# Kernel optimization log

Hardware: AMD Instinct MI355X
Metric: run time of the kernel (lower is better)

Reference implementation:

```python
import jax, jax.numpy as jnp
import numpy as np

BATCH = 2
TIME_N = 196
SPACE_F = 8
D_MODEL = 768
N_HEADS = 12
D_STATE = 16
DT_RANK = 48  # ceil(768/16)
D_CONV = 4
SEQ = 1 + TIME_N * SPACE_F


def _ln(x, w, b, eps=1e-5):
    m = x.mean(-1, keepdims=True)
    v = ((x - m) ** 2).mean(-1, keepdims=True)
    return (x - m) * jax.lax.rsqrt(v + eps) * w + b


def _silu(x):
    return x * jax.nn.sigmoid(x)


def _causal_conv(x, w, b):
    # x: (B, L, d); depthwise causal conv1d, kernel D_CONV, padding left
    L = x.shape[1]
    xp = jnp.pad(x, ((0, 0), (D_CONV - 1, 0), (0, 0)))
    return sum(xp[:, k:k + L, :] * w[:, k] for k in range(D_CONV)) + b


def _ssm(u, delta, A, Bm, C, Dp):
    # u, delta: (B,L,d); A: (d,N); Bm, C: (B,L,N)
    dA = jnp.exp(delta[..., None] * A)                    # (B,L,d,N)
    dBu = (delta * u)[..., None] * Bm[:, :, None, :]      # (B,L,d,N)
    B, L, d, N = dA.shape

    def step(h, inp):
        a, bu = inp
        h = a * h + bu
        return h, h

    _, hs = jax.lax.scan(step, jnp.zeros((B, d, N), dA.dtype),
                         (dA.transpose(1, 0, 2, 3), dBu.transpose(1, 0, 2, 3)))
    return jnp.einsum('lbdn,bln->bld', hs, C) + u * Dp


def _mamba_dir(xp, z, conv_w, conv_b, xproj_w, dt_w, dt_b, A_log, Dp, flip):
    if flip:
        xp = xp[:, ::-1]
        z = z[:, ::-1]
    xc = _silu(_causal_conv(xp, conv_w, conv_b))
    x_dbl = xc @ xproj_w.T
    dt = x_dbl[..., :DT_RANK]
    Bm = x_dbl[..., DT_RANK:DT_RANK + D_STATE]
    C = x_dbl[..., DT_RANK + D_STATE:]
    delta = jax.nn.softplus(dt @ dt_w.T + dt_b)
    y = _ssm(xc, delta, -jnp.exp(A_log), Bm, C, Dp) * _silu(z)
    if flip:
        y = y[:, ::-1]
    return y


def _mamba(x, in_w, cw, cb, xw, dw, db, Al, Dp, cwb, cbb, xwb, dwb, dbb, Alb, Dpb, out_w):
    # bimamba v2: forward scan + backward (flipped) scan, summed, then out_proj
    xz = x @ in_w.T
    xp, z = jnp.split(xz, 2, axis=-1)
    y = (_mamba_dir(xp, z, cw, cb, xw, dw, db, Al, Dp, False)
         + _mamba_dir(xp, z, cwb, cbb, xwb, dwb, dbb, Alb, Dpb, True))
    return y @ out_w.T


def _mha(x, in_w, in_b, out_w, out_b):
    # torch nn.MultiheadAttention default (batch_first=False):
    # x is (L, N, E); attention runs over dim 0 (L), dim 1 (N) is batch.
    L, N, E = x.shape
    hd = E // N_HEADS
    qkv = x @ in_w.T + in_b
    q, k, v = jnp.split(qkv, 3, axis=-1)
    q = q.reshape(L, N, N_HEADS, hd)
    k = k.reshape(L, N, N_HEADS, hd)
    v = v.reshape(L, N, N_HEADS, hd)
    scores = jnp.einsum('lnhk,mnhk->nhlm', q, k) / jnp.sqrt(jnp.asarray(hd, x.dtype))
    o = jnp.einsum('nhlm,mnhk->lnhk', jax.nn.softmax(scores, axis=-1), v)
    return o.reshape(L, N, E) @ out_w.T + out_b


def _forward(x, norm1_w, norm1_b, norm2_w, norm2_b, norm3_w, norm3_b,
             attn_in_w, attn_in_b, attn_out_w, attn_out_b,
             m_in_w, m_conv_w, m_conv_b, m_xproj_w, m_dt_w, m_dt_b, m_Alog, m_D,
             m_conv_wb, m_conv_bb, m_xproj_wb, m_dt_wb, m_dt_bb, m_Alog_b, m_D_b,
             m_out_w, fc1_w, fc1_b, fc2_w, fc2_b, time_n, space_f):
    b, _, d = x.shape
    init_cls = x[:, :1]
    res_x = x
    # 'b (n t) d -> (b n) t d'
    xt = x[:, 1:].reshape(b, time_n, space_f, d).reshape(b * time_n, space_f, d)
    time_out = _mamba(_ln(xt, norm3_w, norm3_b), m_in_w, m_conv_w, m_conv_b,
                      m_xproj_w, m_dt_w, m_dt_b, m_Alog, m_D,
                      m_conv_wb, m_conv_bb, m_xproj_wb, m_dt_wb, m_dt_bb,
                      m_Alog_b, m_D_b, m_out_w)
    time_res = (xt + time_out).reshape(b, time_n, space_f, d)
    # cls repeat: 'b t d -> (b t) 1 d'
    cls = jnp.repeat(init_cls, space_f, axis=1).reshape(b * space_f, 1, d)
    # 'b (n t) d -> (b t) n d'
    xs = time_res.transpose(0, 2, 1, 3).reshape(b * space_f, time_n, d)
    xs = jnp.concatenate([cls, xs], axis=1)  # (b*t, n+1, d)
    space_out = _mha(_ln(xs, norm1_w, norm1_b), attn_in_w, attn_in_b, attn_out_w, attn_out_b)
    cls_tok = space_out[:, 0].reshape(b, space_f, d).mean(1, keepdims=True)
    # '(b t) n d -> b (n t) d'
    sp = space_out[:, 1:].reshape(b, space_f, time_n, d).transpose(0, 2, 1, 3).reshape(b, time_n * space_f, d)
    x = res_x + jnp.concatenate([cls_tok, sp], axis=1)
    h = _ln(x, norm2_w, norm2_b)
    h = jax.nn.gelu(h @ fc1_w.T + fc1_b, approximate=False) @ fc2_w.T + fc2_b
    return x + h


def setup_inputs():
    ks = iter(jax.random.split(jax.random.key(0), 64))

    def nrm(shape, s=0.02):
        return jax.random.normal(next(ks), shape, dtype=jnp.float32) * s

    d = D_MODEL
    Alog = jnp.log(jnp.tile(jnp.arange(1, D_STATE + 1, dtype=jnp.float32), (d, 1)))
    return dict(
        x=jax.random.normal(next(ks), (BATCH, SEQ, d), dtype=jnp.float32),
        norm1_w=jnp.ones((d,), jnp.float32), norm1_b=jnp.zeros((d,), jnp.float32),
        norm2_w=jnp.ones((d,), jnp.float32), norm2_b=jnp.zeros((d,), jnp.float32),
        norm3_w=jnp.ones((d,), jnp.float32), norm3_b=jnp.zeros((d,), jnp.float32),
        attn_in_w=nrm((3 * d, d)), attn_in_b=nrm((3 * d,)),
        attn_out_w=nrm((d, d)), attn_out_b=nrm((d,)),
        m_in_w=nrm((2 * d, d)),
        m_conv_w=nrm((d, D_CONV), 0.2), m_conv_b=nrm((d,), 0.1),
        m_xproj_w=nrm((DT_RANK + 2 * D_STATE, d)),
        m_dt_w=nrm((d, DT_RANK), 0.1), m_dt_b=nrm((d,), 0.5),
        m_Alog=Alog, m_D=jnp.ones((d,), jnp.float32),
        m_conv_wb=nrm((d, D_CONV), 0.2), m_conv_bb=nrm((d,), 0.1),
        m_xproj_wb=nrm((DT_RANK + 2 * D_STATE, d)),
        m_dt_wb=nrm((d, DT_RANK), 0.1), m_dt_bb=nrm((d,), 0.5),
        m_Alog_b=Alog, m_D_b=jnp.ones((d,), jnp.float32),
        m_out_w=nrm((d, d)),
        fc1_w=nrm((4 * d, d)), fc1_b=nrm((4 * d,), 0.01),
        fc2_w=nrm((d, 4 * d)), fc2_b=nrm((d,), 0.01),
        time_n=TIME_N, space_f=SPACE_F,
    )


def reference(x, norm1_w, norm1_b, norm2_w, norm2_b, norm3_w, norm3_b,
              attn_in_w, attn_in_b, attn_out_w, attn_out_b,
              m_in_w, m_conv_w, m_conv_b, m_xproj_w, m_dt_w, m_dt_b, m_Alog, m_D,
              m_conv_wb, m_conv_bb, m_xproj_wb, m_dt_wb, m_dt_bb, m_Alog_b, m_D_b,
              m_out_w, fc1_w, fc1_b, fc2_w, fc2_b, time_n, space_f):
    return _forward(x, norm1_w, norm1_b, norm2_w, norm2_b, norm3_w, norm3_b,
                    attn_in_w, attn_in_b, attn_out_w, attn_out_b,
                    m_in_w, m_conv_w, m_conv_b, m_xproj_w, m_dt_w, m_dt_b, m_Alog, m_D,
                    m_conv_wb, m_conv_bb, m_xproj_wb, m_dt_wb, m_dt_bb, m_Alog_b, m_D_b,
                    m_out_w, fc1_w, fc1_b, fc2_w, fc2_b, time_n, space_f)
```

## Files before the change

kernel.cpp:

```cpp
#include <hip/hip_runtime.h>
#include <hip/hip_bf16.h>
#include <math.h>

#define DM 768
#define NBATCH 2
#define TIMEN 196
#define SPACEF 8
#define SEQL 1569
#define NSTATE 16
#define MT 3136
#define NSEQ 392
#define AT 3152
#define XTOK 3138

typedef __attribute__((ext_vector_type(8))) short s16x8;
typedef __attribute__((ext_vector_type(4))) float f32x4;
typedef __hip_bfloat16 bf16;

__device__ __forceinline__ float silu_fast(float x){ return __fdividef(x, 1.0f + __expf(-x)); }
__device__ __forceinline__ float geluf(float x){
  float y = 0.7978845608f * (x + 0.044715f*x*x*x);
  float ay = fabsf(y);
  float e = __expf(-2.0f*ay);
  float t = __fdividef(1.0f - e, 1.0f + e);
  t = copysignf(t, y);
  return 0.5f*x*(1.0f + t);
}
__device__ __forceinline__ float softplusf(float x){
  return (x > 20.0f) ? x : __logf(1.0f + __expf(x));
}
__device__ __forceinline__ int imin(int a, int b){ return a < b ? a : b; }

#define GLD_LDS16(g, l) __builtin_amdgcn_global_load_lds( \
    (const __attribute__((address_space(1))) void*)(g), \
    (__attribute__((address_space(3))) void*)(l), 16, 0, 0)

template<int N, int K, int Np, int Kp>
__device__ __forceinline__ void cvt_seg(const float* __restrict__ src, bf16* __restrict__ dst){
  const int total = Np * Kp;
  int base = blockIdx.x * 1024 + threadIdx.x;
  #pragma unroll
  for (int e = 0; e < 4; e++){
    int idx = base + e * 256;
    if (idx < total){
      int n = idx / Kp, k = idx % Kp;
      float v = (n < N && k < K) ? src[n * K + k] : 0.0f;
      dst[idx] = __float2bfloat16(v);
    }
  }
}

__global__ __launch_bounds__(256) void cvtw_kernel(
    const float* s0, const float* s1, const float* s2, const float* s3,
    const float* s4, const float* s5, const float* s6, const float* s7,
    const float* s8, const float* s9, bf16* w)
{
  switch (blockIdx.y) {
    case 0: cvt_seg<1536,768,1536,768>(s0, w + 0);        break;
    case 1: cvt_seg<  80,768, 128,768>(s1, w + 1179648);  break;
    case 2: cvt_seg<  80,768, 128,768>(s2, w + 1277952);  break;
    case 3: cvt_seg< 768, 48, 768, 64>(s3, w + 1376256);  break;
    case 4: cvt_seg< 768, 48, 768, 64>(s4, w + 1425408);  break;
    case 5: cvt_seg< 768,768, 768,768>(s5, w + 1474560);  break;
    case 6: cvt_seg<2304,768,2304,768>(s6, w + 2064384);  break;
    case 7: cvt_seg< 768,768, 768,768>(s7, w + 3833856);  break;
    case 8: cvt_seg<3072,768,3072,768>(s8, w + 4423680);  break;
    default:cvt_seg< 768,3072,768,3072>(s9, w + 6782976); break;
  }
}

__device__ __forceinline__ float block_sum256(float v, float* sm){
  #pragma unroll
  for (int o = 32; o > 0; o >>= 1) v += __shfl_down(v, o);
  __syncthreads();
  if ((threadIdx.x & 63) == 0) sm[threadIdx.x >> 6] = v;
  __syncthreads();
  return sm[0] + sm[1] + sm[2] + sm[3];
}

__global__ __launch_bounds__(256) void ln_kernel(
    const float* __restrict__ src0,
    const float* __restrict__ w, const float* __restrict__ b,
    bf16* __restrict__ out)
{
  __shared__ float sm[4];
  int tok = blockIdx.x;
  int bi = tok / (TIMEN*SPACEF), r = tok % (TIMEN*SPACEF);
  const float* src = src0 + ((size_t)bi * SEQL + 1 + r) * DM;
  int tid = threadIdx.x;
  float xr[3];
  #pragma unroll
  for (int i = 0; i < 3; i++) xr[i] = src[tid + i*256];
  float mean = block_sum256(xr[0]+xr[1]+xr[2], sm) * (1.0f/768.0f);
  float v0 = xr[0]-mean, v1 = xr[1]-mean, v2 = xr[2]-mean;
  float var = block_sum256(v0*v0 + v1*v1 + v2*v2, sm) * (1.0f/768.0f);
  float rstd = rsqrtf(var + 1e-5f);
  bf16* o = out + (size_t)tok * DM;
  #pragma unroll
  for (int i = 0; i < 3; i++){ int c = tid + i*256;
    o[c] = __float2bfloat16((xr[i]-mean)*rstd*w[c] + b[c]); }
}

__global__ __launch_bounds__(256) void redk_ln(
    const float* __restrict__ part, const float* __restrict__ x,
    const float* __restrict__ w, const float* __restrict__ b,
    bf16* __restrict__ out)
{
  __shared__ float sm[4];
  int tok = blockIdx.x;
  int sidx = tok / 197, p = tok % 197;
  int tid = threadIdx.x;
  float xr[3];
  if (p == 0) {
    const float* src = x + (size_t)(sidx >> 3) * SEQL * DM;
    #pragma unroll
    for (int i = 0; i < 3; i++) xr[i] = src[tid + i*256];
  } else {
    int bi = sidx >> 3, f = sidx & 7, t = p - 1;
    size_t mt = ((size_t)(bi*TIMEN + t))*SPACEF + f;
    const float* p0 = part + mt*DM;
    const float* p1 = part + ((size_t)MT + mt)*DM;
    const float* xs = x + ((size_t)bi*SEQL + 1 + t*SPACEF + f)*DM;
    #pragma unroll
    for (int i = 0; i < 3; i++){ int c = tid + i*256;
      xr[i] = p0[c] + p1[c] + xs[c]; }
  }
  float mean = block_sum256(xr[0]+xr[1]+xr[2], sm) * (1.0f/768.0f);
  float v0 = xr[0]-mean, v1 = xr[1]-mean, v2 = xr[2]-mean;
  float var = block_sum256(v0*v0 + v1*v1 + v2*v2, sm) * (1.0f/768.0f);
  float rstd = rsqrtf(var + 1e-5f);
  bf16* o = out + (size_t)tok * DM;
  #pragma unroll
  for (int i = 0; i < 3; i++){ int c = tid + i*256;
    o[c] = __float2bfloat16((xr[i]-mean)*rstd*w[c] + b[c]); }
}

__global__ __launch_bounds__(256) void scatter_ln(
    const float* __restrict__ part, const float* __restrict__ bias,
    const float* __restrict__ x, float* __restrict__ xnew,
    const float* __restrict__ w, const float* __restrict__ b,
    bf16* __restrict__ out)
{
  __shared__ float sm[4];
  int tok = blockIdx.x;
  int bi = tok / SEQL, row = tok % SEQL;
  int tid = threadIdx.x;
  const float* p1 = part + (size_t)AT*DM;
  const float* xs = x + (size_t)tok*DM;
  float xr[3];
  if (row == 0) {
    #pragma unroll
    for (int i = 0; i < 3; i++){ int c = tid + i*256;
      float acc = 0.0f;
      #pragma unroll
      for (int f = 0; f < SPACEF; f++){
        size_t r = ((size_t)(bi*SPACEF + f)*197)*DM + c;
        acc += part[r] + p1[r];
      }
      xr[i] = xs[c] + acc * 0.125f + bias[c];
    }
  } else {
    int t = (row - 1) >> 3, f = (row - 1) & 7;
    size_t r = ((size_t)((bi*SPACEF + f)*197) + 1 + t)*DM;
    #pragma unroll
    for (int i = 0; i < 3; i++){ int c = tid + i*256;
      xr[i] = xs[c] + part[r + c] + p1[r + c] + bias[c];
    }
  }
  float* xo = xnew + (size_t)tok*DM;
  #pragma unroll
  for (int i = 0; i < 3; i++) xo[tid + i*256] = xr[i];
  float mean = block_sum256(xr[0]+xr[1]+xr[2], sm) * (1.0f/768.0f);
  float v0 = xr[0]-mean, v1 = xr[1]-mean, v2 = xr[2]-mean;
  float var = block_sum256(v0*v0 + v1*v1 + v2*v2, sm) * (1.0f/768.0f);
  float rstd = rsqrtf(var + 1e-5f);
  bf16* o = out + (size_t)tok*DM;
  #pragma unroll
  for (int i = 0; i < 3; i++){ int c = tid + i*256;
    o[c] = __float2bfloat16((xr[i]-mean)*rstd*w[c] + b[c]); }
}

template<int BM, int BN>
__global__ __launch_bounds__(256) void mgemm(
    const bf16* __restrict__ A, int lda,
    const bf16* __restrict__ W0, const bf16* __restrict__ W1, int ldw,
    const float* __restrict__ bias0, const float* __restrict__ bias1,
    const float* __restrict__ resid,
    void* __restrict__ Cout, int M, int mhalf, int N, int ldc, int KP,
    int act, int resmode, int outbf16, int skw)
{
  constexpr int WM = BM/2, WN = BN/2, MI = WM/16, NJ = WN/16;
  __shared__ bf16 As[2][BM*64];
  __shared__ bf16 Bs[2][BN*64];
  int tid = threadIdx.x;
  int wave = tid >> 6, lane = tid & 63;

  int gx = gridDim.x, gy = gridDim.y;
  int nwg = gx * gy;
  int bid = blockIdx.y * gx + blockIdx.x;
  int m0, n0;
  if ((gx & 3) == 0 && (gy & 1) == 0) {
    int cw = gx >> 2, rh = gy >> 1;
    int xcd = bid & 7, lidx = bid >> 3;
    int rx = xcd & 3, ry = xcd >> 2;
    m0 = ((ry * rh) + lidx / cw) * BM;
    n0 = ((rx * cw) + lidx % cw) * BN;
  } else {
    int q = nwg >> 3, r = nwg & 7;
    int xcd = bid & 7, lidx = bid >> 3;
    int wg = (xcd < r ? xcd*(q+1) : r*(q+1) + (xcd-r)*q) + lidx;
    m0 = (wg / gx) * BM; n0 = (wg % gx) * BN;
  }

  int wr = wave >> 1, wc = wave & 1;

  int koff = blockIdx.z * KP;
  const bf16* Ak = A + koff;
  const bf16* Wt = ((m0 < mhalf) ? W0 : W1) + koff;
  const float* bias = (m0 < mhalf) ? bias0 : bias1;

  f32x4 acc[MI][NJ];
  #pragma unroll
  for (int i = 0; i < MI; i++)
    #pragma unroll
    for (int j = 0; j < NJ; j++) acc[i][j] = (f32x4){0.f,0.f,0.f,0.f};

  int sr8 = lane >> 3;
  int scs = (((lane & 7) ^ sr8) * 8);
  int lr16 = lane & 15, ks = (lane >> 4) * 8;
  int swz = (lr16 & 7) << 3;

  auto stage = [&](int buf, int k0){
    #pragma unroll
    for (int g = 0; g < BM/32; g++){
      int rr = wave*(BM/4) + g*8;
      const bf16* ga = Ak + (size_t)imin(m0 + rr + sr8, M-1)*lda + k0 + scs;
      GLD_LDS16(ga, &As[buf][rr*64]);
    }
    #pragma unroll
    for (int g = 0; g < BN/32; g++){
      int rr = wave*(BN/4) + g*8;
      const bf16* gb = Wt + (size_t)(n0 + rr + sr8)*ldw + k0 + scs;
      GLD_LDS16(gb, &Bs[buf][rr*64]);
    }
  };

  auto compute = [&](int buf){
    s16x8 afr[2][MI], bfr[2][NJ];
    #pragma unroll
    for (int kk = 0; kk < 2; kk++){
      #pragma unroll
      for (int i = 0; i < MI; i++)
        afr[kk][i] = *(const s16x8*)&As[buf][(wr*WM + i*16 + lr16)*64 + ((kk*32 + ks) ^ swz)];
      #pragma unroll
      for (int j = 0; j < NJ; j++)
        bfr[kk][j] = *(const s16x8*)&Bs[buf][(wc*WN + j*16 + lr16)*64 + ((kk*32 + ks) ^ swz)];
    }
    #pragma unroll
    for (int kk = 0; kk < 2; kk++)
      #pragma unroll
      for (int i = 0; i < MI; i++)
        #pragma unroll
        for (int j = 0; j < NJ; j++)
          acc[i][j] = __builtin_amdgcn_mfma_f32_16x16x32_bf16(afr[kk][i], bfr[kk][j], acc[i][j], 0, 0, 0);
  };

  stage(0, 0);
  __syncthreads();
  int cur = 0;
  for (int k0 = 64; k0 < KP; k0 += 64){
    stage(cur ^ 1, k0);
    compute(cur);
    __syncthreads();
    cur ^= 1;
  }
  compute(cur);

  #pragma unroll
  for (int i = 0; i < MI; i++){
    int rowb = m0 + wr*WM + i*16 + (lane >> 4)*4;
    #pragma unroll
    for (int j = 0; j < NJ; j++){
      int col = n0 + wc*WN + j*16 + lr16;
      if (col >= N) continue;
      float bv = bias ? bias[col] : 0.0f;
      #pragma unroll
      for (int r2 = 0; r2 < 4; r2++){
        int row = rowb + r2;
        if (row >= M) continue;
        float v = acc[i][j][r2];
        if (skw > 1){
          ((float*)Cout)[((size_t)(blockIdx.z*M) + row)*ldc + col] = v;
          continue;
        }
        v += bv;
        if (act == 1) v = geluf(v);
        else if (act == 2) v = softplusf(v);
        if (resmode == 1) v += resid[(size_t)row*ldc + col];
        if (outbf16) ((bf16*)Cout)[(size_t)row*ldc + col] = __float2bfloat16(v);
        else         ((float*)Cout)[(size_t)row*ldc + col] = v;
      }
    }
  }
}

__global__ __launch_bounds__(256) void redk(
    const float* __restrict__ part, const float* __restrict__ bias,
    const float* __restrict__ resid, float* __restrict__ out,
    int M, int sk)
{
  int i = blockIdx.x*256 + threadIdx.x;
  if (i*4 >= M*768) return;
  int row = i / 192;
  int c4 = (i - row*192) * 4;
  size_t base = (size_t)row*768 + c4;
  float4 v = *(const float4*)(part + base);
  for (int z = 1; z < sk; z++){
    float4 p = *(const float4*)(part + (size_t)z*M*768 + base);
    v.x += p.x; v.y += p.y; v.z += p.z; v.w += p.w;
  }
  float4 bvec = *(const float4*)(bias + c4);
  float4 r = *(const float4*)(resid + base);
  v.x += bvec.x + r.x; v.y += bvec.y + r.y; v.z += bvec.z + r.z; v.w += bvec.w + r.w;
  *(float4*)(out + base) = v;
}

__global__ __launch_bounds__(256) void conv_kernel(
    const float* __restrict__ xz,
    const float* __restrict__ wf, const float* __restrict__ bf,
    const float* __restrict__ wb, const float* __restrict__ bb,
    bf16* __restrict__ xcf, bf16* __restrict__ xcb)
{
  int g = blockIdx.x*256 + threadIdx.x;
  if (g >= NSEQ*DM) return;
  int s = g / DM, d = g % DM;
  float xr[8];
  #pragma unroll
  for (int j = 0; j < 8; j++) xr[j] = xz[(size_t)(s*8 + j)*1536 + d];
  float wfv[4], wbv[4];
  #pragma unroll
  for (int k = 0; k < 4; k++){ wfv[k] = wf[d*4+k]; wbv[k] = wb[d*4+k]; }
  float bfv = bf[d], bbv = bb[d];
  #pragma unroll
  for (int l = 0; l < 8; l++) {
    float af = bfv, ab = bbv;
    #pragma unroll
    for (int k = 0; k < 4; k++) {
      if (l + k >= 3) {
        af += wfv[k] * xr[l + k - 3];
        ab += wbv[k] * xr[10 - l - k];
      }
    }
    xcf[(size_t)(s*8 + l)*DM + d] = __float2bfloat16(silu_fast(af));
    xcb[(size_t)(s*8 + l)*DM + d] = __float2bfloat16(silu_fast(ab));
  }
}

__global__ __launch_bounds__(256) void ssm_kernel(
    const float* __restrict__ xz,
    const bf16* __restrict__ xcf, const bf16* __restrict__ xcb,
    const bf16* __restrict__ dblf, const bf16* __restrict__ dblb,
    const bf16* __restrict__ dlf, const bf16* __restrict__ dlb,
    const float* __restrict__ Alogf, const float* __restrict__ Df,
    const float* __restrict__ Alogb, const float* __restrict__ Db,
    bf16* __restrict__ y)
{
  int s = blockIdx.y;
  int d = blockIdx.x*256 + threadIdx.x;
  int tid = threadIdx.x;
  __shared__ float sBC[2][8][32];
  #pragma unroll
  for (int i = 0; i < 2; i++){
    int idx = tid + i*256;
    int dir = idx >> 8, r = idx & 255, l = r >> 5, j = r & 31;
    const bf16* p = dir ? dblb : dblf;
    sBC[dir][l][j] = __bfloat162float(p[(size_t)(s*8 + l)*80 + 48 + j]);
  }
  float Af[NSTATE], Ab[NSTATE];
  #pragma unroll
  for (int n = 0; n < NSTATE; n++) {
    Af[n] = -__expf(Alogf[d*NSTATE + n]);
    Ab[n] = -__expf(Alogb[d*NSTATE + n]);
  }
  float Dfv = Df[d], Dbv = Db[d];
  __syncthreads();

  float hf[NSTATE] = {}, hb[NSTATE] = {};
  float yf[8], yb[8];
  #pragma unroll
  for (int l = 0; l < 8; l++) {
    int t = s*8 + l;
    float delf = __bfloat162float(dlf[(size_t)t*DM + d]);
    float uf   = __bfloat162float(xcf[(size_t)t*DM + d]);
    float duf  = delf * uf;
    float accf = 0.0f;
    #pragma unroll
    for (int n = 0; n < NSTATE; n++) {
      hf[n] = __expf(delf*Af[n])*hf[n] + duf*sBC[0][l][n];
      accf += hf[n]*sBC[0][l][16+n];
    }
    yf[l] = accf + uf*Dfv;
    float delb = __bfloat162float(dlb[(size_t)t*DM + d]);
    float ub   = __bfloat162float(xcb[(size_t)t*DM + d]);
    float dub  = delb * ub;
    float accb = 0.0f;
    #pragma unroll
    for (int n = 0; n < NSTATE; n++) {
      hb[n] = __expf(delb*Ab[n])*hb[n] + dub*sBC[1][l][n];
      accb += hb[n]*sBC[1][l][16+n];
    }
    yb[7-l] = accb + ub*Dbv;
  }
  #pragma unroll
  for (int l = 0; l < 8; l++) {
    int t = s*8 + l;
    float zv = xz[(size_t)t*1536 + DM + d];
    y[(size_t)t*DM + d] = __float2bfloat16((yf[l] + yb[l]) * silu_fast(zv));
  }
}

__global__ __launch_bounds__(256) void attn_kernel(
    const bf16* __restrict__ qkv, bf16* __restrict__ ao)
{
  int n = blockIdx.x / 12, h = blockIdx.x % 12;
  __shared__ float qs[16][65], ks[16][65], vs[16][65], ps[16][17];
  int tid = threadIdx.x;
  for (int e = tid; e < 1024; e += 256) {
    int l = e >> 6, c = e & 63;
    size_t row = ((size_t)l*197 + n)*2304 + h*64 + c;
    qs[l][c] = __bfloat162float(qkv[row]);
    ks[l][c] = __bfloat162float(qkv[row + 768]);
    vs[l][c] = __bfloat162float(qkv[row + 1536]);
  }
  __syncthreads();
  int l = tid >> 4, m = tid & 15;
  float sc = 0.0f;
  #pragma unroll
  for (int c = 0; c < 64; c++) sc += qs[l][c]*ks[m][c];
  sc *= 0.125f;
  float mx = sc;
  #pragma unroll
  for (int o = 8; o > 0; o >>= 1) mx = fmaxf(mx, __shfl_xor(mx, o, 16));
  float p = __expf(sc - mx);
  float smv = p;
  #pragma unroll
  for (int o = 8; o > 0; o >>= 1) smv += __shfl_xor(smv, o, 16);
  ps[l][m] = __fdividef(p, smv);
  __syncthreads();
  for (int e = tid; e < 1024; e += 256) {
    int ll = e >> 6, c = e & 63;
    float acc = 0.0f;
    #pragma unroll
    for (int mm = 0; mm < 16; mm++) acc += ps[ll][mm]*vs[mm][c];
    ao[((size_t)ll*197 + n)*768 + h*64 + c] = __float2bfloat16(acc);
  }
}

extern "C" void kernel_launch(void* const* d_in, const int* in_sizes, int n_in,
                              void* d_out, int out_size, void* d_ws, size_t ws_size,
                              hipStream_t stream) {
  const float* x        = (const float*)d_in[0];
  const float* norm1_w  = (const float*)d_in[1];
  const float* norm1_b  = (const float*)d_in[2];
  const float* norm2_w  = (const float*)d_in[3];
  const float* norm2_b  = (const float*)d_in[4];
  const float* norm3_w  = (const float*)d_in[5];
  const float* norm3_b  = (const float*)d_in[6];
  const float* attn_in_w  = (const float*)d_in[7];
  const float* attn_in_b  = (const float*)d_in[8];
  const float* attn_out_w = (const float*)d_in[9];
  const float* attn_out_b = (const float*)d_in[10];
  const float* m_in_w   = (const float*)d_in[11];
  const float* m_conv_w = (const float*)d_in[12];
  const float* m_conv_b = (const float*)d_in[13];
  const float* m_xproj_w= (const float*)d_in[14];
  const float* m_dt_w   = (const float*)d_in[15];
  const float* m_dt_b   = (const float*)d_in[16];
  const float* m_Alog   = (const float*)d_in[17];
  const float* m_D      = (const float*)d_in[18];
  const float* m_conv_wb= (const float*)d_in[19];
  const float* m_conv_bb= (const float*)d_in[20];
  const float* m_xproj_wb=(const float*)d_in[21];
  const float* m_dt_wb  = (const float*)d_in[22];
  const float* m_dt_bb  = (const float*)d_in[23];
  const float* m_Alog_b = (const float*)d_in[24];
  const float* m_D_b    = (const float*)d_in[25];
  const float* m_out_w  = (const float*)d_in[26];
  const float* fc1_w    = (const float*)d_in[27];
  const float* fc1_b    = (const float*)d_in[28];
  const float* fc2_w    = (const float*)d_in[29];
  const float* fc2_b    = (const float*)d_in[30];

  char* wsb = (char*)d_ws;
  bf16*  wpool  = (bf16*)(wsb + 0);
  bf16*  ln3    = (bf16*)(wsb + 18284544);
  float* xz     = (float*)(wsb + 23101440);
  bf16*  xcf    = (bf16*)(wsb + 42369024);
  bf16*  xcb    = (bf16*)(wsb + 47185920);
  bf16*  dblf   = (bf16*)(wsb + 52002816);
  bf16*  dblb   = (bf16*)(wsb + 52504576);
  bf16*  dlf    = (bf16*)(wsb + 53006336);
  bf16*  dlb    = (bf16*)(wsb + 57823232);
  bf16*  y      = ln3;
  float* part1  = (float*)(wsb + 23101440);
  bf16*  xsln   = (bf16*)(wsb + 62640128);
  bf16*  qkv    = (bf16*)(wsb + 42369024);
  bf16*  ao     = (bf16*)(wsb + 18284544);
  float* part2  = (float*)(wsb + 42369024);
  float* xnew   = (float*)(wsb + 62640128);
  bf16*  ln2o   = (bf16*)(wsb + 23101440);
  bf16*  h1     = (bf16*)(wsb + 42369024);
  float* part3  = (float*)(wsb + 18284544);

  bf16* w_in  = wpool + 0;
  bf16* w_xpf = wpool + 1179648;
  bf16* w_xpb = wpool + 1277952;
  bf16* w_dtf = wpool + 1376256;
  bf16* w_dtb = wpool + 1425408;
  bf16* w_out = wpool + 1474560;
  bf16* w_qkv = wpool + 2064384;
  bf16* w_ao  = wpool + 3833856;
  bf16* w_fc1 = wpool + 4423680;
  bf16* w_fc2 = wpool + 6782976;

  const int BIGM = 1 << 30;

  cvtw_kernel<<<dim3(2304, 10), 256, 0, stream>>>(
      m_in_w, m_xproj_w, m_xproj_wb, m_dt_w, m_dt_wb, m_out_w,
      attn_in_w, attn_out_w, fc1_w, fc2_w, wpool);

  ln_kernel<<<MT, 256, 0, stream>>>(x, norm3_w, norm3_b, ln3);
  mgemm<64,64><<<dim3(24, 49), 256, 0, stream>>>(ln3, DM, w_in, w_in, DM,
      nullptr, nullptr, nullptr, xz, MT, BIGM, 1536, 1536, DM, 0, 0, 0, 1);
  conv_kernel<<<(NSEQ*DM + 255)/256, 256, 0, stream>>>(
      xz, m_conv_w, m_conv_b, m_conv_wb, m_conv_bb, xcf, xcb);
  mgemm<64,64><<<dim3(2, 98), 256, 0, stream>>>(xcf, DM, w_xpf, w_xpb, DM,
      nullptr, nullptr, nullptr, dblf, 2*MT, MT, 80, 80, DM, 0, 0, 1, 1);
  mgemm<64,64><<<dim3(12, 98), 256, 0, stream>>>(dblf, 80, w_dtf, w_dtb, 64,
      m_dt_b, m_dt_bb, nullptr, dlf, 2*MT, MT, DM, DM, 64, 2, 0, 1, 1);
  ssm_kernel<<<dim3(3, NSEQ), 256, 0, stream>>>(
      xz, xcf, xcb, dblf, dblb, dlf, dlb, m_Alog, m_D, m_Alog_b, m_D_b, y);
  mgemm<64,64><<<dim3(12, 49, 2), 256, 0, stream>>>(y, DM, w_out, w_out, DM,
      nullptr, nullptr, nullptr, part1, MT, BIGM, DM, DM, 384, 0, 0, 0, 2);

  redk_ln<<<AT, 256, 0, stream>>>(part1, x, norm1_w, norm1_b, xsln);
  mgemm<64,64><<<dim3(36, 50), 256, 0, stream>>>(xsln, DM, w_qkv, w_qkv, DM,
      attn_in_b, attn_in_b, nullptr, qkv, AT, BIGM, 2304, 2304, DM, 0, 0, 1, 1);
  attn_kernel<<<197*12, 256, 0, stream>>>(qkv, ao);
  mgemm<64,64><<<dim3(12, 50, 2), 256, 0, stream>>>(ao, DM, w_ao, w_ao, DM,
      nullptr, nullptr, nullptr, part2, AT, BIGM, DM, DM, 384, 0, 0, 0, 2);

  scatter_ln<<<XTOK, 256, 0, stream>>>(part2, attn_out_b, x, xnew,
      norm2_w, norm2_b, ln2o);
  mgemm<64,64><<<dim3(48, 50), 256, 0, stream>>>(ln2o, DM, w_fc1, w_fc1, DM,
      fc1_b, fc1_b, nullptr, h1, XTOK, BIGM, 3072, 3072, DM, 1, 0, 1, 1);
  mgemm<64,64><<<dim3(12, 50, 2), 256, 0, stream>>>(h1, 3072, w_fc2, w_fc2, 3072,
      nullptr, nullptr, nullptr, part3, XTOK, BIGM, DM, DM, 1536, 0, 0, 0, 2);
  redk<<<2354, 256, 0, stream>>>(part3, fc2_b, xnew, (float*)d_out, XTOK, 2);
}
```

Before: 269.9 us.

## Add 64x128 two-wave GEMM kernel with K=32 steps for large projections

```diff
diff --git a/kernel.cpp b/kernel.cpp
--- a/kernel.cpp
+++ b/kernel.cpp
@@ -185,13 +185,114 @@
     const bf16* __restrict__ A, int lda,
     const bf16* __restrict__ W0, const bf16* __restrict__ W1, int ldw,
     const float* __restrict__ bias0, const float* __restrict__ bias1,
-    const float* __restrict__ resid,
     void* __restrict__ Cout, int M, int mhalf, int N, int ldc, int KP,
-    int act, int resmode, int outbf16, int skw)
+    int act, int outbf16)
 {
   constexpr int WM = BM/2, WN = BN/2, MI = WM/16, NJ = WN/16;
   __shared__ bf16 As[2][BM*64];
   __shared__ bf16 Bs[2][BN*64];
+  int tid = threadIdx.x;
+  int wave = tid >> 6, lane = tid & 63;
+
+  int gx = gridDim.x;
+  int nwg = gx * gridDim.y;
+  int bid = blockIdx.y * gx + blockIdx.x;
+  int q = nwg >> 3, r = nwg & 7;
+  int xcd = bid & 7, lidx = bid >> 3;
+  int wg = (xcd < r ? xcd*(q+1) : r*(q+1) + (xcd-r)*q) + lidx;
+  int m0 = (wg / gx) * BM, n0 = (wg % gx) * BN;
+
+  int wr = wave >> 1, wc = wave & 1;
+  const bf16* Wt = ((m0 < mhalf) ? W0 : W1);
+  const float* bias = (m0 < mhalf) ? bias0 : bias1;
+
+  f32x4 acc[MI][NJ];
+  #pragma unroll
+  for (int i = 0; i < MI; i++)
+    #pragma unroll
+    for (int j = 0; j < NJ; j++) acc[i][j] = (f32x4){0.f,0.f,0.f,0.f};
+
+  int sr8 = lane >> 3;
+  int scs = (((lane & 7) ^ sr8) * 8);
+  int lr16 = lane & 15, ks = (lane >> 4) * 8;
+  int swz = (lr16 & 7) << 3;
+
+  auto stage = [&](int buf, int k0){
+    #pragma unroll
+    for (int g = 0; g < BM/32; g++){
+      int rr = wave*(BM/4) + g*8;
+      const bf16* ga = A + (size_t)imin(m0 + rr + sr8, M-1)*lda + k0 + scs;
+      GLD_LDS16(ga, &As[buf][rr*64]);
+    }
+    #pragma unroll
+    for (int g = 0; g < BN/32; g++){
+      int rr = wave*(BN/4) + g*8;
+      const bf16* gb = Wt + (size_t)(n0 + rr + sr8)*ldw + k0 + scs;
+      GLD_LDS16(gb, &Bs[buf][rr*64]);
+    }
+  };
+
+  auto compute = [&](int buf){
+    s16x8 afr[2][MI], bfr[2][NJ];
+    #pragma unroll
+    for (int kk = 0; kk < 2; kk++){
+      #pragma unroll
+      for (int i = 0; i < MI; i++)
+        afr[kk][i] = *(const s16x8*)&As[buf][(wr*WM + i*16 + lr16)*64 + ((kk*32 + ks) ^ swz)];
+      #pragma unroll
+      for (int j = 0; j < NJ; j++)
+        bfr[kk][j] = *(const s16x8*)&Bs[buf][(wc*WN + j*16 + lr16)*64 + ((kk*32 + ks) ^ swz)];
+    }
+    #pragma unroll
+    for (int kk = 0; kk < 2; kk++)
+      #pragma unroll
+      for (int i = 0; i < MI; i++)
+        #pragma unroll
+        for (int j = 0; j < NJ; j++)
+          acc[i][j] = __builtin_amdgcn_mfma_f32_16x16x32_bf16(afr[kk][i], bfr[kk][j], acc[i][j], 0, 0, 0);
+  };
+
+  stage(0, 0);
+  __syncthreads();
+  int cur = 0;
+  for (int k0 = 64; k0 < KP; k0 += 64){
+    stage(cur ^ 1, k0);
+    compute(cur);
+    __syncthreads();
+    cur ^= 1;
+  }
+  compute(cur);
+
+  #pragma unroll
+  for (int i = 0; i < MI; i++){
+    int rowb = m0 + wr*WM + i*16 + (lane >> 4)*4;
+    #pragma unroll
+    for (int j = 0; j < NJ; j++){
+      int col = n0 + wc*WN + j*16 + lr16;
+      if (col >= N) continue;
+      float bv = bias ? bias[col] : 0.0f;
+      #pragma unroll
+      for (int r2 = 0; r2 < 4; r2++){
+        int row = rowb + r2;
+        if (row >= M) continue;
+        float v = acc[i][j][r2] + bv;
+        if (act == 2) v = softplusf(v);
+        if (outbf16) ((bf16*)Cout)[(size_t)row*ldc + col] = __float2bfloat16(v);
+        else         ((float*)Cout)[(size_t)row*ldc + col] = v;
+      }
+    }
+  }
+}
+
+__global__ __launch_bounds__(128) void mgemm2(
+    const bf16* __restrict__ A, int lda,
+    const bf16* __restrict__ W0, int ldw,
+    const float* __restrict__ bias0,
+    void* __restrict__ Cout, int M, int N, int ldc, int KP,
+    int act, int outbf16, int skw)
+{
+  __shared__ bf16 As[2][64*32];
+  __shared__ bf16 Bs[2][128*32];
   int tid = threadIdx.x;
   int wave = tid >> 6, lane = tid & 63;
 
@@ -203,72 +304,64 @@
     int cw = gx >> 2, rh = gy >> 1;
     int xcd = bid & 7, lidx = bid >> 3;
     int rx = xcd & 3, ry = xcd >> 2;
-    m0 = ((ry * rh) + lidx / cw) * BM;
-    n0 = ((rx * cw) + lidx % cw) * BN;
+    m0 = ((ry * rh) + lidx / cw) * 64;
+    n0 = ((rx * cw) + lidx % cw) * 128;
   } else {
     int q = nwg >> 3, r = nwg & 7;
     int xcd = bid & 7, lidx = bid >> 3;
     int wg = (xcd < r ? xcd*(q+1) : r*(q+1) + (xcd-r)*q) + lidx;
-    m0 = (wg / gx) * BM; n0 = (wg % gx) * BN;
-  }
-
-  int wr = wave >> 1, wc = wave & 1;
+    m0 = (wg / gx) * 64; n0 = (wg % gx) * 128;
+  }
 
   int koff = blockIdx.z * KP;
   const bf16* Ak = A + koff;
-  const bf16* Wt = ((m0 < mhalf) ? W0 : W1) + koff;
-  const float* bias = (m0 < mhalf) ? bias0 : bias1;
-
-  f32x4 acc[MI][NJ];
-  #pragma unroll
-  for (int i = 0; i < MI; i++)
-    #pragma unroll
-    for (int j = 0; j < NJ; j++) acc[i][j] = (f32x4){0.f,0.f,0.f,0.f};
-
-  int sr8 = lane >> 3;
-  int scs = (((lane & 7) ^ sr8) * 8);
+  const bf16* Wt = W0 + koff;
+
+  f32x4 acc[4][4];
+  #pragma unroll
+  for (int i = 0; i < 4; i++)
+    #pragma unroll
+    for (int j = 0; j < 4; j++) acc[i][j] = (f32x4){0.f,0.f,0.f,0.f};
+
+  int srow = lane >> 2;
+  int scs = ((lane & 3) ^ ((lane >> 3) & 3)) * 8;
   int lr16 = lane & 15, ks = (lane >> 4) * 8;
-  int swz = (lr16 & 7) << 3;
+  int swz = ((lr16 >> 1) & 3) << 3;
 
   auto stage = [&](int buf, int k0){
     #pragma unroll
-    for (int g = 0; g < BM/32; g++){
-      int rr = wave*(BM/4) + g*8;
-      const bf16* ga = Ak + (size_t)imin(m0 + rr + sr8, M-1)*lda + k0 + scs;
-      GLD_LDS16(ga, &As[buf][rr*64]);
-    }
-    #pragma unroll
-    for (int g = 0; g < BN/32; g++){
-      int rr = wave*(BN/4) + g*8;
-      const bf16* gb = Wt + (size_t)(n0 + rr + sr8)*ldw + k0 + scs;
-      GLD_LDS16(gb, &Bs[buf][rr*64]);
+    for (int g = 0; g < 2; g++){
+      int rb = g*32 + wave*16;
+      const bf16* ga = Ak + (size_t)imin(m0 + rb + srow, M-1)*lda + k0 + scs;
+      GLD_LDS16(ga, &As[buf][rb*32]);
+    }
+    #pragma unroll
+    for (int g = 0; g < 4; g++){
+      int rb = g*32 + wave*16;
+      const bf16* gb = Wt + (size_t)(n0 + rb + srow)*ldw + k0 + scs;
+      GLD_LDS16(gb, &Bs[buf][rb*32]);
     }
   };
 
   auto compute = [&](int buf){
-    s16x8 afr[2][MI], bfr[2][NJ];
-    #pragma unroll
-    for (int kk = 0; kk < 2; kk++){
+    s16x8 afr[4], bfr[4];
+    #pragma unroll
+    for (int i = 0; i < 4; i++)
+      afr[i] = *(const s16x8*)&As[buf][(i*16 + lr16)*32 + (ks ^ swz)];
+    #pragma unroll
+    for (int j = 0; j < 4; j++)
+      bfr[j] = *(const s16x8*)&Bs[buf][(wave*64 + j*16 + lr16)*32 + (ks ^ swz)];
+    #pragma unroll
+    for (int i = 0; i < 4; i++)
       #pragma unroll
-      for (int i = 0; i < MI; i++)
-        afr[kk][i] = *(const s16x8*)&As[buf][(wr*WM + i*16 + lr16)*64 + ((kk*32 + ks) ^ swz)];
-      #pragma unroll
-      for (int j = 0; j < NJ; j++)
-        bfr[kk][j] = *(const s16x8*)&Bs[buf][(wc*WN + j*16 + lr16)*64 + ((kk*32 + ks) ^ swz)];
-    }
-    #pragma unroll
-    for (int kk = 0; kk < 2; kk++)
-      #pragma unroll
-      for (int i = 0; i < MI; i++)
-        #pragma unroll
-        for (int j = 0; j < NJ; j++)
-          acc[i][j] = __builtin_amdgcn_mfma_f32_16x16x32_bf16(afr[kk][i], bfr[kk][j], acc[i][j], 0, 0, 0);
+      for (int j = 0; j < 4; j++)
+        acc[i][j] = __builtin_amdgcn_mfma_f32_16x16x32_bf16(afr[i], bfr[j], acc[i][j], 0, 0, 0);
   };
 
   stage(0, 0);
   __syncthreads();
   int cur = 0;
-  for (int k0 = 64; k0 < KP; k0 += 64){
+  for (int k0 = 32; k0 < KP; k0 += 32){
     stage(cur ^ 1, k0);
     compute(cur);
     __syncthreads();
@@ -277,13 +370,13 @@
   compute(cur);
 
   #pragma unroll
-  for (int i = 0; i < MI; i++){
-    int rowb = m0 + wr*WM + i*16 + (lane >> 4)*4;
-    #pragma unroll
-    for (int j = 0; j < NJ; j++){
-      int col = n0 + wc*WN + j*16 + lr16;
+  for (int i = 0; i < 4; i++){
+    int rowb = m0 + i*16 + (lane >> 4)*4;
+    #pragma unroll
+    for (int j = 0; j < 4; j++){
+      int col = n0 + wave*64 + j*16 + lr16;
       if (col >= N) continue;
-      float bv = bias ? bias[col] : 0.0f;
+      float bv = bias0 ? bias0[col] : 0.0f;
       #pragma unroll
       for (int r2 = 0; r2 < 4; r2++){
         int row = rowb + r2;
@@ -295,8 +388,6 @@
         }
         v += bv;
         if (act == 1) v = geluf(v);
-        else if (act == 2) v = softplusf(v);
-        if (resmode == 1) v += resid[(size_t)row*ldc + col];
         if (outbf16) ((bf16*)Cout)[(size_t)row*ldc + col] = __float2bfloat16(v);
         else         ((float*)Cout)[(size_t)row*ldc + col] = v;
       }
@@ -530,31 +621,31 @@
       attn_in_w, attn_out_w, fc1_w, fc2_w, wpool);
 
   ln_kernel<<<MT, 256, 0, stream>>>(x, norm3_w, norm3_b, ln3);
-  mgemm<64,64><<<dim3(24, 49), 256, 0, stream>>>(ln3, DM, w_in, w_in, DM,
-      nullptr, nullptr, nullptr, xz, MT, BIGM, 1536, 1536, DM, 0, 0, 0, 1);
+  mgemm2<<<dim3(12, 49), 128, 0, stream>>>(ln3, DM, w_in, DM,
+      nullptr, xz, MT, 1536, 1536, DM, 0, 0, 1);
   conv_kernel<<<(NSEQ*DM + 255)/256, 256, 0, stream>>>(
       xz, m_conv_w, m_conv_b, m_conv_wb, m_conv_bb, xcf, xcb);
   mgemm<64,64><<<dim3(2, 98), 256, 0, stream>>>(xcf, DM, w_xpf, w_xpb, DM,
-      nullptr, nullptr, nullptr, dblf, 2*MT, MT, 80, 80, DM, 0, 0, 1, 1);
+      nullptr, nullptr, dblf, 2*MT, MT, 80, 80, DM, 0, 1);
   mgemm<64,64><<<dim3(12, 98), 256, 0, stream>>>(dblf, 80, w_dtf, w_dtb, 64,
-      m_dt_b, m_dt_bb, nullptr, dlf, 2*MT, MT, DM, DM, 64, 2, 0, 1, 1);
+      m_dt_b, m_dt_bb, dlf, 2*MT, MT, DM, DM, 64, 2, 1);
   ssm_kernel<<<dim3(3, NSEQ), 256, 0, stream>>>(
       xz, xcf, xcb, dblf, dblb, dlf, dlb, m_Alog, m_D, m_Alog_b, m_D_b, y);
-  mgemm<64,64><<<dim3(12, 49, 2), 256, 0, stream>>>(y, DM, w_out, w_out, DM,
-      nullptr, nullptr, nullptr, part1, MT, BIGM, DM, DM, 384, 0, 0, 0, 2);
+  mgemm2<<<dim3(6, 49, 2), 128, 0, stream>>>(y, DM, w_out, DM,
+      nullptr, part1, MT, DM, DM, 384, 0, 0, 2);
 
   redk_ln<<<AT, 256, 0, stream>>>(part1, x, norm1_w, norm1_b, xsln);
-  mgemm<64,64><<<dim3(36, 50), 256, 0, stream>>>(xsln, DM, w_qkv, w_qkv, DM,
-      attn_in_b, attn_in_b, nullptr, qkv, AT, BIGM, 2304, 2304, DM, 0, 0, 1, 1);
+  mgemm2<<<dim3(18, 50), 128, 0, stream>>>(xsln, DM, w_qkv, DM,
+      attn_in_b, qkv, AT, 2304, 2304, DM, 0, 1, 1);
   attn_kernel<<<197*12, 256, 0, stream>>>(qkv, ao);
-  mgemm<64,64><<<dim3(12, 50, 2), 256, 0, stream>>>(ao, DM, w_ao, w_ao, DM,
-      nullptr, nullptr, nullptr, part2, AT, BIGM, DM, DM, 384, 0, 0, 0, 2);
+  mgemm2<<<dim3(6, 50, 2), 128, 0, stream>>>(ao, DM, w_ao, DM,
+      nullptr, part2, AT, DM, DM, 384, 0, 0, 2);
 
   scatter_ln<<<XTOK, 256, 0, stream>>>(part2, attn_out_b, x, xnew,
       norm2_w, norm2_b, ln2o);
-  mgemm<64,64><<<dim3(48, 50), 256, 0, stream>>>(ln2o, DM, w_fc1, w_fc1, DM,
-      fc1_b, fc1_b, nullptr, h1, XTOK, BIGM, 3072, 3072, DM, 1, 0, 1, 1);
-  mgemm<64,64><<<dim3(12, 50, 2), 256, 0, stream>>>(h1, 3072, w_fc2, w_fc2, 3072,
-      nullptr, nullptr, nullptr, part3, XTOK, BIGM, DM, DM, 1536, 0, 0, 0, 2);
+  mgemm2<<<dim3(24, 50), 128, 0, stream>>>(ln2o, DM, w_fc1, DM,
+      fc1_b, h1, XTOK, 3072, 3072, DM, 1, 1, 1);
+  mgemm2<<<dim3(6, 50, 2), 128, 0, stream>>>(h1, 3072, w_fc2, 3072,
+      nullptr, part3, XTOK, DM, DM, 1536, 0, 0, 2);
   redk<<<2354, 256, 0, stream>>>(part3, fc2_b, xnew, (float*)d_out, XTOK, 2);
 }
```

Measured after the change: 312.2 us. +15.7%, slower.
